# Kernel tuning notes

Hardware: AMD Instinct MI355X
Metric: run time of the kernel (lower is better)

Reference implementation:

```python
import jax, jax.numpy as jnp
import numpy as np

N, M, D, U = 4096, 65536, 64, 4  # samples, manifold pts, embed dim, manifold coord dim


def setup_inputs() -> dict:
    key = jax.random.key(0)
    k1, k2, k3, k4 = jax.random.split(key, 4)
    return {
        "X": jax.random.normal(k1, (N, D), dtype=jnp.float32),
        "manifold_ptsX": jax.random.normal(k2, (M, D), dtype=jnp.float32),
        # per-manifold-point first derivatives d sigma / d u_i : [M, U, D]
        "d_ui_sigma": jax.random.normal(k3, (M, U, D), dtype=jnp.float32),
        # per-manifold-point second derivatives d^2 sigma / d u_i d u_j : [M, U, U, D]
        "d_ui_uj_sigma": jax.random.normal(k4, (M, U, U, D), dtype=jnp.float32),
    }


def _nearest_idx(X, pts):
    # Brute-force 1-NN in squared euclidean distance (replaces CPU sklearn KDTree query).
    # but we keep it for exactness of the distance values.
    d2 = (jnp.sum(X * X, axis=1, keepdims=True)
          - 2.0 * (X @ pts.T)
          + jnp.sum(pts * pts, axis=1)[None, :])  # [N, M]
    return jnp.argmin(d2, axis=1)  # [N]


def reference(X, manifold_ptsX, d_ui_sigma, d_ui_uj_sigma):
    # Forward: project each input point to its nearest manifold point.
    I_x = _nearest_idx(X, manifold_ptsX)          # [N]
    x = manifold_ptsX[I_x, :]                     # [N, D]
    return x
```

## Files before the change

kernel.cpp:

```cpp
#include <hip/hip_runtime.h>
#include <math.h>
#include <stdint.h>

#define NQ 4096
#define MP 65536
#define DD 64
#define QT 64
#define STRIPES 8
#define PPB (MP / STRIPES)
#define GPS (PPB / 16)
#define PGROUPS (MP / 16)
#define XGROUPS (NQ / 16)

typedef _Float16 f16;
typedef _Float16 f16x8 __attribute__((ext_vector_type(8)));
typedef float f32x4 __attribute__((ext_vector_type(4)));


__global__ __launch_bounds__(256) void prep_k(const float* __restrict__ P,
                                              const float* __restrict__ X,
                                              f16* __restrict__ PF,
                                              f16* __restrict__ XF,
                                              float* __restrict__ pnh) {
    const int w = threadIdx.x >> 6, lane = threadIdx.x & 63;
    const int n16 = lane & 15, quad = lane >> 4;
    const int task = blockIdx.x * 4 + w;
    const float* src; f16* dst; int g; bool dopn;
    if (task < PGROUPS) { src = P; dst = PF; g = task; dopn = true; }
    else                { src = X; dst = XF; g = task - PGROUPS; dopn = false; }

    const float* row = src + ((size_t)g * 16 + n16) * DD;
    float ss = 0.f;
    #pragma unroll
    for (int kh = 0; kh < 2; ++kh) {
        float4 v0 = *reinterpret_cast<const float4*>(row + kh * 32 + quad * 8);
        float4 v1 = *reinterpret_cast<const float4*>(row + kh * 32 + quad * 8 + 4);
        float vv[8] = {v0.x, v0.y, v0.z, v0.w, v1.x, v1.y, v1.z, v1.w};
        f16x8 h, l;
        #pragma unroll
        for (int j = 0; j < 8; ++j) {
            f16 hh = (f16)vv[j];
            h[j] = hh;
            l[j] = (f16)(vv[j] - (float)hh);
            ss = fmaf(vv[j], vv[j], ss);
        }
        *reinterpret_cast<f16x8*>(dst + ((size_t)(g * 2 + 0) * 2 + kh) * 512 + lane * 8) = h;
        *reinterpret_cast<f16x8*>(dst + ((size_t)(g * 2 + 1) * 2 + kh) * 512 + lane * 8) = l;
    }
    if (dopn) {
        ss += __shfl_xor(ss, 16);
        ss += __shfl_xor(ss, 32);
        if (quad == 0) pnh[g * 16 + n16] = 0.5f * ss;
    }
}

__global__ __launch_bounds__(256, 2) void argmin_k(const f16* __restrict__ PF,
                                                   const f16* __restrict__ XF,
                                                   const float* __restrict__ pnh,
                                                   unsigned long long* __restrict__ best) {
    const int t = threadIdx.x;
    const int lane = t & 63, w = t >> 6;
    const int n16 = lane & 15, quad = lane >> 4;
    const int b = blockIdx.x;
    const int stripe = b & 7;
    const int qBase = (b >> 3) * QT;

    f16x8 QH[4][2], QL[4][2];
    {
        const int qg0 = qBase >> 4;
        #pragma unroll
        for (int nt = 0; nt < 4; ++nt)
            #pragma unroll
            for (int kh = 0; kh < 2; ++kh) {
                const f16* o = XF + ((size_t)(qg0 + nt) * 4 + kh) * 512 + lane * 8;
                QH[nt][kh] = *reinterpret_cast<const f16x8*>(o);
                QL[nt][kh] = *reinterpret_cast<const f16x8*>(o + 1024);
            }
    }

    float rmax[4];
    int   ridx[4];
    #pragma unroll
    for (int nt = 0; nt < 4; ++nt) { rmax[nt] = -INFINITY; ridx[nt] = 0; }

    auto PROC = [&](int gg, f16x8* PH, f16x8* PL) {
        f32x4 pq = *reinterpret_cast<const f32x4*>(pnh + gg * 16 + quad * 4);
        #pragma unroll
        for (int nt = 0; nt < 4; ++nt) {
            f32x4 a = {0.f, 0.f, 0.f, 0.f};
            #pragma unroll
            for (int kh = 0; kh < 2; ++kh) {
                a = __builtin_amdgcn_mfma_f32_16x16x32_f16(PH[kh], QH[nt][kh], a, 0, 0, 0);
                a = __builtin_amdgcn_mfma_f32_16x16x32_f16(PH[kh], QL[nt][kh], a, 0, 0, 0);
                a = __builtin_amdgcn_mfma_f32_16x16x32_f16(PL[kh], QH[nt][kh], a, 0, 0, 0);
            }
            float s0 = a[0] - pq[0], s1 = a[1] - pq[1];
            float s2 = a[2] - pq[2], s3 = a[3] - pq[3];
            float smax = fmaxf(fmaxf(s0, s1), fmaxf(s2, s3));
            if (smax > rmax[nt]) {
                rmax[nt] = smax;
                int r = 3;
                r = (s2 == smax) ? 2 : r;
                r = (s1 == smax) ? 1 : r;
                r = (s0 == smax) ? 0 : r;
                ridx[nt] = gg * 16 + quad * 4 + r;
            }
        }
    };

    int g = stripe * GPS + w;
    f16x8 PHa[2], PLa[2], PHb[2], PLb[2];
    {
        const f16* f0 = PF + (size_t)g * 2048 + lane * 8;
        PHa[0] = *reinterpret_cast<const f16x8*>(f0);
        PHa[1] = *reinterpret_cast<const f16x8*>(f0 + 512);
        PLa[0] = *reinterpret_cast<const f16x8*>(f0 + 1024);
        PLa[1] = *reinterpret_cast<const f16x8*>(f0 + 1536);
    }
    for (int i = 0; i < GPS / 4; i += 2) {
        {
            const f16* fn = PF + (size_t)(g + 4) * 2048 + lane * 8;
            PHb[0] = *reinterpret_cast<const f16x8*>(fn);
            PHb[1] = *reinterpret_cast<const f16x8*>(fn + 512);
            PLb[0] = *reinterpret_cast<const f16x8*>(fn + 1024);
            PLb[1] = *reinterpret_cast<const f16x8*>(fn + 1536);
        }
        PROC(g, PHa, PLa);
        {
            int gp = (i + 2 < GPS / 4) ? g + 8 : g;
            const f16* fn = PF + (size_t)gp * 2048 + lane * 8;
            PHa[0] = *reinterpret_cast<const f16x8*>(fn);
            PHa[1] = *reinterpret_cast<const f16x8*>(fn + 512);
            PLa[0] = *reinterpret_cast<const f16x8*>(fn + 1024);
            PLa[1] = *reinterpret_cast<const f16x8*>(fn + 1536);
        }
        PROC(g + 4, PHb, PLb);
        g += 8;
    }

    #pragma unroll
    for (int nt = 0; nt < 4; ++nt) {
        float sv = rmax[nt]; int iv = ridx[nt];
        #pragma unroll
        for (int m = 16; m < 64; m <<= 1) {
            float so = __shfl_xor(sv, m);
            int   io = __shfl_xor(iv, m);
            if (so > sv || (so == sv && io < iv)) { sv = so; iv = io; }
        }
        if (quad == 0) {
            float s = -2.f * sv;
            unsigned u = __float_as_uint(s);
            u = (u & 0x80000000u) ? ~u : (u | 0x80000000u);
            unsigned long long key = ((unsigned long long)u << 32) | (unsigned)iv;
            atomicMin(&best[qBase + nt * 16 + n16], key);
        }
    }
}

__global__ __launch_bounds__(256) void gather_k(const unsigned long long* __restrict__ best,
                                                const float* __restrict__ P,
                                                float* __restrict__ out) {
    int g = blockIdx.x * 256 + threadIdx.x;
    int q = g >> 4, c = g & 15;
    unsigned idx = (unsigned)best[q];
    reinterpret_cast<float4*>(out)[g] =
        reinterpret_cast<const float4*>(P)[(size_t)idx * 16 + c];
}

extern "C" void kernel_launch(void* const* d_in, const int* in_sizes, int n_in,
                              void* d_out, int out_size, void* d_ws, size_t ws_size,
                              hipStream_t stream) {
    const float* X = (const float*)d_in[0];
    const float* P = (const float*)d_in[1];
    float* out = (float*)d_out;

    unsigned long long* best = (unsigned long long*)d_ws;
    float* pnh = (float*)((char*)d_ws + 32768);
    f16*   XF  = (f16*)((char*)d_ws + 294912);
    f16*   PF  = (f16*)((char*)d_ws + 1343488);

    hipMemsetAsync(d_ws, 0xFF, NQ * sizeof(unsigned long long), stream);

    prep_k<<<(PGROUPS + XGROUPS) / 4, 256, 0, stream>>>(P, X, PF, XF, pnh);

    argmin_k<<<(NQ / QT) * STRIPES, 256, 0, stream>>>(PF, XF, pnh, best);

    gather_k<<<NQ * 16 / 256, 256, 0, stream>>>(best, P, out);
}
```

Baseline: 419.6 us.

## Switch nearest-neighbor scoring from 16x16x32 to 32x32x16 MFMA tiles

Repacks the split-f16 (hi/lo) point and query fragments into 32-row groups and computes the dot-product scores with 32x32x16 MFMA instructions instead of 16x16x32. Each wave now processes 32 points by 64 queries per step, which halves the number of candidate groups per stripe and reduces per-element argmin bookkeeping and cross-lane reductions. In exchange it uses larger accumulator (16 floats) and operand register footprints, which may pressure occupancy under the 2-blocks launch bound.

After: 431.7 us. +2.9%, slower.

```diff
diff --git a/kernel.cpp b/kernel.cpp
--- a/kernel.cpp
+++ b/kernel.cpp
@@ -8,13 +8,14 @@
 #define QT 64
 #define STRIPES 8
 #define PPB (MP / STRIPES)
-#define GPS (PPB / 16)
-#define PGROUPS (MP / 16)
-#define XGROUPS (NQ / 16)
+#define GPS (PPB / 32)
+#define PG32 (MP / 32)
+#define XG32 (NQ / 32)
 
 typedef _Float16 f16;
 typedef _Float16 f16x8 __attribute__((ext_vector_type(8)));
 typedef float f32x4 __attribute__((ext_vector_type(4)));
+typedef float f32x16 __attribute__((ext_vector_type(16)));
 
 
 __global__ __launch_bounds__(256) void prep_k(const float* __restrict__ P,
@@ -23,18 +24,19 @@
                                               f16* __restrict__ XF,
                                               float* __restrict__ pnh) {
     const int w = threadIdx.x >> 6, lane = threadIdx.x & 63;
-    const int n16 = lane & 15, quad = lane >> 4;
+    const int r32 = lane & 31, hw = lane >> 5;
     const int task = blockIdx.x * 4 + w;
     const float* src; f16* dst; int g; bool dopn;
-    if (task < PGROUPS) { src = P; dst = PF; g = task; dopn = true; }
-    else                { src = X; dst = XF; g = task - PGROUPS; dopn = false; }
+    if (task < PG32) { src = P; dst = PF; g = task; dopn = true; }
+    else             { src = X; dst = XF; g = task - PG32; dopn = false; }
 
-    const float* row = src + ((size_t)g * 16 + n16) * DD;
+    const float* row = src + ((size_t)g * 32 + r32) * DD;
     float ss = 0.f;
     #pragma unroll
-    for (int kh = 0; kh < 2; ++kh) {
-        float4 v0 = *reinterpret_cast<const float4*>(row + kh * 32 + quad * 8);
-        float4 v1 = *reinterpret_cast<const float4*>(row + kh * 32 + quad * 8 + 4);
+    for (int ks = 0; ks < 4; ++ks) {
+        const float* p0 = row + ks * 16 + hw * 8;
+        float4 v0 = *reinterpret_cast<const float4*>(p0);
+        float4 v1 = *reinterpret_cast<const float4*>(p0 + 4);
         float vv[8] = {v0.x, v0.y, v0.z, v0.w, v1.x, v1.y, v1.z, v1.w};
         f16x8 h, l;
         #pragma unroll
@@ -44,13 +46,13 @@
             l[j] = (f16)(vv[j] - (float)hh);
             ss = fmaf(vv[j], vv[j], ss);
         }
-        *reinterpret_cast<f16x8*>(dst + ((size_t)(g * 2 + 0) * 2 + kh) * 512 + lane * 8) = h;
-        *reinterpret_cast<f16x8*>(dst + ((size_t)(g * 2 + 1) * 2 + kh) * 512 + lane * 8) = l;
+        f16* base = dst + ((size_t)(g * 2 + 0) * 4 + ks) * 512 + lane * 8;
+        *reinterpret_cast<f16x8*>(base) = h;
+        *reinterpret_cast<f16x8*>(base + 2048) = l;
     }
     if (dopn) {
-        ss += __shfl_xor(ss, 16);
         ss += __shfl_xor(ss, 32);
-        if (quad == 0) pnh[g * 16 + n16] = 0.5f * ss;
+        if (hw == 0) pnh[g * 32 + r32] = 0.5f * ss;
     }
 }
 
@@ -60,99 +62,102 @@
                                                    unsigned long long* __restrict__ best) {
     const int t = threadIdx.x;
     const int lane = t & 63, w = t >> 6;
-    const int n16 = lane & 15, quad = lane >> 4;
+    const int c32 = lane & 31, hw = lane >> 5;
     const int b = blockIdx.x;
     const int stripe = b & 7;
-    const int qBase = (b >> 3) * QT;
+    const int qt = b >> 3;
+    const int qBase = qt * QT;
 
-    f16x8 QH[4][2], QL[4][2];
-    {
-        const int qg0 = qBase >> 4;
+    f16x8 QH[2][4], QL[2][4];
+    #pragma unroll
+    for (int nt = 0; nt < 2; ++nt)
         #pragma unroll
-        for (int nt = 0; nt < 4; ++nt)
+        for (int ks = 0; ks < 4; ++ks) {
+            const f16* o = XF + ((size_t)((qt * 2 + nt) * 2 + 0) * 4 + ks) * 512 + lane * 8;
+            QH[nt][ks] = *reinterpret_cast<const f16x8*>(o);
+            QL[nt][ks] = *reinterpret_cast<const f16x8*>(o + 2048);
+        }
+
+    float rmax[2];
+    int   ridx[2];
+    #pragma unroll
+    for (int nt = 0; nt < 2; ++nt) { rmax[nt] = -INFINITY; ridx[nt] = 0; }
+
+    auto PROC = [&](int gg, f16x8* FH, f16x8* FL) {
+        f32x4 pq[4];
+        #pragma unroll
+        for (int i = 0; i < 4; ++i)
+            pq[i] = *reinterpret_cast<const f32x4*>(pnh + gg * 32 + i * 8 + hw * 4);
+        #pragma unroll
+        for (int nt = 0; nt < 2; ++nt) {
+            f32x16 a = {0.f,0.f,0.f,0.f,0.f,0.f,0.f,0.f,0.f,0.f,0.f,0.f,0.f,0.f,0.f,0.f};
             #pragma unroll
-            for (int kh = 0; kh < 2; ++kh) {
-                const f16* o = XF + ((size_t)(qg0 + nt) * 4 + kh) * 512 + lane * 8;
-                QH[nt][kh] = *reinterpret_cast<const f16x8*>(o);
-                QL[nt][kh] = *reinterpret_cast<const f16x8*>(o + 1024);
+            for (int ks = 0; ks < 4; ++ks) {
+                a = __builtin_amdgcn_mfma_f32_32x32x16_f16(FH[ks], QH[nt][ks], a, 0, 0, 0);
+                a = __builtin_amdgcn_mfma_f32_32x32x16_f16(FH[ks], QL[nt][ks], a, 0, 0, 0);
+                a = __builtin_amdgcn_mfma_f32_32x32x16_f16(FL[ks], QH[nt][ks], a, 0, 0, 0);
             }
-    }
-
-    float rmax[4];
-    int   ridx[4];
-    #pragma unroll
-    for (int nt = 0; nt < 4; ++nt) { rmax[nt] = -INFINITY; ridx[nt] = 0; }
-
-    auto PROC = [&](int gg, f16x8* PH, f16x8* PL) {
-        f32x4 pq = *reinterpret_cast<const f32x4*>(pnh + gg * 16 + quad * 4);
-        #pragma unroll
-        for (int nt = 0; nt < 4; ++nt) {
-            f32x4 a = {0.f, 0.f, 0.f, 0.f};
+            float s[16];
             #pragma unroll
-            for (int kh = 0; kh < 2; ++kh) {
-                a = __builtin_amdgcn_mfma_f32_16x16x32_f16(PH[kh], QH[nt][kh], a, 0, 0, 0);
-                a = __builtin_amdgcn_mfma_f32_16x16x32_f16(PH[kh], QL[nt][kh], a, 0, 0, 0);
-                a = __builtin_amdgcn_mfma_f32_16x16x32_f16(PL[kh], QH[nt][kh], a, 0, 0, 0);
-            }
-            float s0 = a[0] - pq[0], s1 = a[1] - pq[1];
-            float s2 = a[2] - pq[2], s3 = a[3] - pq[3];
-            float smax = fmaxf(fmaxf(s0, s1), fmaxf(s2, s3));
+            for (int r = 0; r < 16; ++r) s[r] = a[r] - pq[r >> 2][r & 3];
+            float smax = s[0];
+            #pragma unroll
+            for (int r = 1; r < 16; ++r) smax = fmaxf(smax, s[r]);
             if (smax > rmax[nt]) {
                 rmax[nt] = smax;
-                int r = 3;
-                r = (s2 == smax) ? 2 : r;
-                r = (s1 == smax) ? 1 : r;
-                r = (s0 == smax) ? 0 : r;
-                ridx[nt] = gg * 16 + quad * 4 + r;
+                int rr = 15;
+                #pragma unroll
+                for (int r = 14; r >= 0; --r) rr = (s[r] == smax) ? r : rr;
+                ridx[nt] = gg * 32 + (rr & 3) + 8 * (rr >> 2) + 4 * hw;
             }
         }
     };
 
     int g = stripe * GPS + w;
-    f16x8 PHa[2], PLa[2], PHb[2], PLb[2];
+    f16x8 HA[4], LA[4], HB[4], LB[4];
     {
-        const f16* f0 = PF + (size_t)g * 2048 + lane * 8;
-        PHa[0] = *reinterpret_cast<const f16x8*>(f0);
-        PHa[1] = *reinterpret_cast<const f16x8*>(f0 + 512);
-        PLa[0] = *reinterpret_cast<const f16x8*>(f0 + 1024);
-        PLa[1] = *reinterpret_cast<const f16x8*>(f0 + 1536);
+        const f16* f0 = PF + (size_t)g * 4096 + lane * 8;
+        #pragma unroll
+        for (int ks = 0; ks < 4; ++ks) {
+            HA[ks] = *reinterpret_cast<const f16x8*>(f0 + ks * 512);
+            LA[ks] = *reinterpret_cast<const f16x8*>(f0 + 2048 + ks * 512);
+        }
     }
-    for (int i = 0; i < GPS / 4; i += 2) {
+    for (int i = 0; i < GPS / 8; ++i) {
         {
-            const f16* fn = PF + (size_t)(g + 4) * 2048 + lane * 8;
-            PHb[0] = *reinterpret_cast<const f16x8*>(fn);
-            PHb[1] = *reinterpret_cast<const f16x8*>(fn + 512);
-            PLb[0] = *reinterpret_cast<const f16x8*>(fn + 1024);
-            PLb[1] = *reinterpret_cast<const f16x8*>(fn + 1536);
+            const f16* fn = PF + (size_t)(g + 4) * 4096 + lane * 8;
+            #pragma unroll
+            for (int ks = 0; ks < 4; ++ks) {
+                HB[ks] = *reinterpret_cast<const f16x8*>(fn + ks * 512);
+                LB[ks] = *reinterpret_cast<const f16x8*>(fn + 2048 + ks * 512);
+            }
         }
-        PROC(g, PHa, PLa);
+        PROC(g, HA, LA);
         {
-            int gp = (i + 2 < GPS / 4) ? g + 8 : g;
-            const f16* fn = PF + (size_t)gp * 2048 + lane * 8;
-            PHa[0] = *reinterpret_cast<const f16x8*>(fn);
-            PHa[1] = *reinterpret_cast<const f16x8*>(fn + 512);
-            PLa[0] = *reinterpret_cast<const f16x8*>(fn + 1024);
-            PLa[1] = *reinterpret_cast<const f16x8*>(fn + 1536);
+            int gp = (i + 1 < GPS / 8) ? g + 8 : g;
+            const f16* fn = PF + (size_t)gp * 4096 + lane * 8;
+            #pragma unroll
+            for (int ks = 0; ks < 4; ++ks) {
+                HA[ks] = *reinterpret_cast<const f16x8*>(fn + ks * 512);
+                LA[ks] = *reinterpret_cast<const f16x8*>(fn + 2048 + ks * 512);
+            }
         }
-        PROC(g + 4, PHb, PLb);
+        PROC(g + 4, HB, LB);
         g += 8;
     }
 
     #pragma unroll
-    for (int nt = 0; nt < 4; ++nt) {
+    for (int nt = 0; nt < 2; ++nt) {
         float sv = rmax[nt]; int iv = ridx[nt];
-        #pragma unroll
-        for (int m = 16; m < 64; m <<= 1) {
-            float so = __shfl_xor(sv, m);
-            int   io = __shfl_xor(iv, m);
-            if (so > sv || (so == sv && io < iv)) { sv = so; iv = io; }
-        }
-        if (quad == 0) {
+        float so = __shfl_xor(sv, 32);
+        int   io = __shfl_xor(iv, 32);
+        if (so > sv || (so == sv && io < iv)) { sv = so; iv = io; }
+        if (hw == 0) {
             float s = -2.f * sv;
             unsigned u = __float_as_uint(s);
             u = (u & 0x80000000u) ? ~u : (u | 0x80000000u);
             unsigned long long key = ((unsigned long long)u << 32) | (unsigned)iv;
-            atomicMin(&best[qBase + nt * 16 + n16], key);
+            atomicMin(&best[qBase + nt * 32 + c32], key);
         }
     }
 }
@@ -181,7 +186,7 @@
 
     hipMemsetAsync(d_ws, 0xFF, NQ * sizeof(unsigned long long), stream);
 
-    prep_k<<<(PGROUPS + XGROUPS) / 4, 256, 0, stream>>>(P, X, PF, XF, pnh);
+    prep_k<<<(PG32 + XG32) / 4, 256, 0, stream>>>(P, X, PF, XF, pnh);
 
     argmin_k<<<(NQ / QT) * STRIPES, 256, 0, stream>>>(PF, XF, pnh, best);
 
```
